# Performance work log

Hardware: AMD Instinct MI355X
Metric: run time of the kernel (lower is better)

Reference implementation:

```python
import jax, jax.numpy as jnp
import numpy as np

B, T, D, H, OUT_STEPS = 4096, 50, 64, 128, 100  # batch, warmup steps, latent dim, hidden units, rollout steps


def setup_inputs() -> dict:
    key = jax.random.key(0)
    ks = jax.random.split(key, 9)
    s = jnp.float32(0.05)  # keep gates out of saturation
    return {
        "x":   jax.random.normal(ks[0], (B, T, D), jnp.float32),
        "Wk0": jax.random.normal(ks[1], (D, 4 * H), jnp.float32) * s,
        "Wr0": jax.random.normal(ks[2], (H, 4 * H), jnp.float32) * s,
        "b0":  jax.random.normal(ks[3], (4 * H,), jnp.float32) * s,
        "Wk1": jax.random.normal(ks[4], (H, 4 * H), jnp.float32) * s,
        "Wr1": jax.random.normal(ks[5], (H, 4 * H), jnp.float32) * s,
        "b1":  jax.random.normal(ks[6], (4 * H,), jnp.float32) * s,
        "Wd":  jax.random.normal(ks[7], (H, D), jnp.float32) * s,
        "bd":  jax.random.normal(ks[8], (D,), jnp.float32) * s,
    }


def _lstm_cell(xt, h, c, Wk, Wr, b):
    # Keras LSTMCell: gates in order i, f, g(cell), o
    z = xt @ Wk + h @ Wr + b  # [B, 4H]
    i, f, g, o = jnp.split(z, 4, axis=-1)
    c_new = jax.nn.sigmoid(f) * c + jax.nn.sigmoid(i) * jnp.tanh(g)
    h_new = jax.nn.sigmoid(o) * jnp.tanh(c_new)
    return h_new, c_new


def reference(x, Wk0, Wr0, b0, Wk1, Wr1, b1, Wd, bd):
    Bn = x.shape[0]
    Hn = Wr0.shape[0]
    z = jnp.zeros((Bn, Hn), x.dtype)

    def warm_step(carry, xt):
        h0, c0, h1, c1 = carry
        h0, c0 = _lstm_cell(xt, h0, c0, Wk0, Wr0, b0)
        h1, c1 = _lstm_cell(h0, h1, c1, Wk1, Wr1, b1)
        return (h0, c0, h1, c1), None

    # warmup over the provided sequence (T >= min_warmup_steps=10)
    carry, _ = jax.lax.scan(warm_step, (z, z, z, z), jnp.swapaxes(x, 0, 1))
    pred0 = carry[2] @ Wd + bd  # Dense on last layer's hidden state

    def ar_step(carry, _):
        pred, h0, c0, h1, c1 = carry
        h0, c0 = _lstm_cell(pred, h0, c0, Wk0, Wr0, b0)
        h1, c1 = _lstm_cell(h0, h1, c1, Wk1, Wr1, b1)
        pred = h1 @ Wd + bd
        return (pred, h0, c0, h1, c1), pred

    _, preds = jax.lax.scan(ar_step, (pred0,) + carry, None, length=OUT_STEPS - 1)
    preds = jnp.concatenate([pred0[None], preds], axis=0)  # [OUT, B, D]
    return jnp.swapaxes(preds, 0, 1)  # [B, OUT, D]
```

## Files before the change

kernel.cpp:

```cpp
#include <hip/hip_runtime.h>
#include <hip/hip_bf16.h>

#define Tt   50
#define Dd   64
#define NOUT 100
#define G4   512
#define K0S  72
#define K1P  264
#define BM   16

typedef __attribute__((ext_vector_type(8))) short  short8;
typedef __attribute__((ext_vector_type(4))) float  floatx4;

#if __has_builtin(__builtin_amdgcn_exp2f)
#define EXP2(v) __builtin_amdgcn_exp2f(v)
#else
#define EXP2(v) exp2f(v)
#endif
__device__ __forceinline__ float rcp_(float v) { return __builtin_amdgcn_rcpf(v); }
#define KN2L2E (-2.8853900817779268f)

#define BARRIER() asm volatile("s_waitcnt lgkmcnt(0)\n\ts_barrier" ::: "memory")

__device__ __forceinline__ short f2bf(float f) {
    __hip_bfloat16 h = __float2bfloat16(f);
    return *reinterpret_cast<const short*>(&h);
}

#define W1F_OFF 196608
#define WDF_OFF 458752
#define B0F_OFF 475136
#define B1F_OFF 477184
#define BDF_OFF 479232

__global__ __launch_bounds__(256) void prep_kernel(
    const float* __restrict__ Wk0, const float* __restrict__ Wr0, const float* __restrict__ b0,
    const float* __restrict__ Wk1, const float* __restrict__ Wr1, const float* __restrict__ b1,
    const float* __restrict__ Wd,  const float* __restrict__ bd,  char* __restrict__ ws)
{
    int idx = blockIdx.x * 256 + threadIdx.x;
    short* w0f = (short*)ws;
    short* w1f = (short*)(ws + W1F_OFF);
    short* wdf = (short*)(ws + WDF_OFF);
    float* b0f = (float*)(ws + B0F_OFF);
    float* b1f = (float*)(ws + B1F_OFF);
    float* bdf = (float*)(ws + BDF_OFF);
    const float NL2E = -1.4426950408889634f;
    const float N2L2E = -2.8853900817779268f;

    if (idx < 98304) {
        int f = idx >> 9, r = idx & 511;
        int lane = r >> 3, j = r & 7;
        int nt = f / 6, kt = f - nt * 6;
        int k = kt * 32 + (lane >> 4) * 8 + j;
        int col = nt * 16 + (lane & 15);
        float sc = ((col >> 7) == 2) ? N2L2E : NL2E;
        w0f[idx] = f2bf(sc * ((k < Dd) ? Wk0[k * G4 + col] : Wr0[(k - Dd) * G4 + col]));
    } else if (idx < 229376) {
        int i2 = idx - 98304;
        int f = i2 >> 9, r = i2 & 511;
        int lane = r >> 3, j = r & 7;
        int nt = f >> 3, kt = f & 7;
        int k = kt * 32 + (lane >> 4) * 8 + j;
        int col = nt * 16 + (lane & 15);
        float sc = ((col >> 7) == 2) ? N2L2E : NL2E;
        w1f[i2] = f2bf(sc * ((k < 128) ? Wk1[k * G4 + col] : Wr1[(k - 128) * G4 + col]));
    } else if (idx < 237568) {
        int i2 = idx - 229376;
        int f = i2 >> 9, r = i2 & 511;
        int lane = r >> 3, j = r & 7;
        int nt = f >> 2, kt = f & 3;
        int k = kt * 32 + (lane >> 4) * 8 + j;
        int col = nt * 16 + (lane & 15);
        wdf[i2] = f2bf(Wd[k * Dd + col]);
    } else if (idx < 237568 + 1088) {
        int i2 = idx - 237568;
        if (i2 < 512) {
            float sc = ((i2 >> 7) == 2) ? N2L2E : NL2E;
            b0f[i2] = sc * b0[i2];
        } else if (i2 < 1024) {
            int c = i2 - 512;
            float sc = ((c >> 7) == 2) ? N2L2E : NL2E;
            b1f[c] = sc * b1[c];
        } else bdf[i2 - 1024] = bd[i2 - 1024];
    }
}

#define SM_A1  4608
#define SM_W0  21504
#define SM_TOT 152576
#define A0SZ   1152
#define A1SZ   4224

#define MFMA_B16(A, B, C) __builtin_amdgcn_mfma_f32_16x16x32_bf16((A), (B), (C), 0, 0, 0)

#define GATES(ACC, CS, BASE, COLOFF)                                                     \
    _Pragma("unroll")                                                                    \
    for (int rr = 0; rr < 4; ++rr) {                                                     \
        float Ei = EXP2(ACC[0][rr]);                                                     \
        float Ef = EXP2(ACC[1][rr]);                                                     \
        float Eg = EXP2(ACC[2][rr]);                                                     \
        float Eo = EXP2(ACC[3][rr]);                                                     \
        float ig = (1.0f - Eg) * rcp_((1.0f + Ei) * (1.0f + Eg));                        \
        float c_ = fmaf(rcp_(1.0f + Ef), CS[rr], ig);                                    \
        CS[rr] = c_;                                                                     \
        float Ec = EXP2(c_ * KN2L2E);                                                    \
        float h_ = (1.0f - Ec) * rcp_((1.0f + Eo) * (1.0f + Ec));                        \
        (BASE)[(quad * 4 + rr) * K1P + (COLOFF) + hu] = f2bf(h_);                        \
    }

__global__ __launch_bounds__(512, 2) void lstm_kernel(
    const float* __restrict__ x, const char* __restrict__ ws, float* __restrict__ out)
{
    extern __shared__ char smem[];
    short* a0b = (short*)smem;
    short* a1b = (short*)(smem + SM_A1);
    short* w0l = (short*)(smem + SM_W0);

    const short* w0f = (const short*)ws;
    const short* w1f = (const short*)(ws + W1F_OFF);
    const short* wdf = (const short*)(ws + WDF_OFF);
    const float* b0f = (const float*)(ws + B0F_OFF);
    const float* b1f = (const float*)(ws + B1F_OFF);
    const float* bdf = (const float*)(ws + BDF_OFF);

    const int tid  = threadIdx.x;
    const int w    = tid >> 6;
    const int lane = tid & 63;
    const int l15  = lane & 15;
    const int quad = lane >> 4;
    const int row0 = blockIdx.x * BM;

    for (int i = tid; i < 2 * A0SZ; i += 512) a0b[i] = 0;
    for (int i = tid; i < 2 * A1SZ; i += 512) a1b[i] = 0;
    for (int c = tid; c < 8192; c += 512) {
        int e8 = c & 63;
        int wv = (c >> 6) & 7;
        int p  = c >> 9;
        int g = p / 6, kt = p - g * 6;
        const short* src = w0f + ((((g * 8 + wv) * 6) + kt) << 9) + e8 * 8;
        *(short8*)&w0l[((p * 8 + wv) << 9) + e8 * 8] = *(const short8*)src;
    }
    {
        int colx = tid & 63, rg = tid >> 6;
        a0b[rg * K0S + colx]       = f2bf(x[(size_t)(row0 + rg) * (Tt * Dd) + colx]);
        a0b[(rg + 8) * K0S + colx] = f2bf(x[(size_t)(row0 + rg + 8) * (Tt * Dd) + colx]);
    }

    const short* w0rb = w0f + w * 3072 + lane * 8;
    const short* w1rb = w1f + w * 4096 + lane * 8;
    short8 W1R[4][8];
    #pragma unroll
    for (int g = 0; g < 4; ++g)
        #pragma unroll
        for (int kt = 0; kt < 8; ++kt)
            W1R[g][kt] = *(const short8*)(w1rb + g * 32768 + kt * 512);
    short8 W0R[8];
    #pragma unroll
    for (int p = 16; p < 24; ++p) {
        int g = p / 6, kt = p - g * 6;
        W0R[p - 16] = *(const short8*)(w0rb + g * 24576 + kt * 512);
    }
    short8 WdR[4];
    if (w < 4) {
        #pragma unroll
        for (int kt = 0; kt < 4; ++kt)
            WdR[kt] = *(const short8*)(wdf + ((w * 4 + kt) << 9) + lane * 8);
    }

    const int hu = w * 16 + l15;
    const float bi0 = b0f[hu], bff0 = b0f[128 + hu], bg0 = b0f[256 + hu], bo0 = b0f[384 + hu];
    const float bi1 = b1f[hu], bff1 = b1f[128 + hu], bg1 = b1f[256 + hu], bo1 = b1f[384 + hu];
    const float bdv = bdf[(w & 3) * 16 + l15];

    float c0s[4] = {0.f, 0.f, 0.f, 0.f};
    float c1s[4] = {0.f, 0.f, 0.f, 0.f};

    const int colx = tid & 63, rg = tid >> 6;

    __syncthreads();

    for (int step = 0; step < 149; ++step) {
        const int p = step & 1, q = p ^ 1;
        short* a0p = a0b + p * A0SZ;  short* a0q = a0b + q * A0SZ;
        short* a1p = a1b + p * A1SZ;  short* a1q = a1b + q * A1SZ;

        float xv0, xv1;
        if (step < Tt - 1) {
            xv0 = x[(size_t)(row0 + rg)     * (Tt * Dd) + (step + 1) * Dd + colx];
            xv1 = x[(size_t)(row0 + rg + 8) * (Tt * Dd) + (step + 1) * Dd + colx];
        }

        floatx4 acc[4];
        acc[0] = (floatx4){bi0,  bi0,  bi0,  bi0};
        acc[1] = (floatx4){bff0, bff0, bff0, bff0};
        acc[2] = (floatx4){bg0,  bg0,  bg0,  bg0};
        acc[3] = (floatx4){bo0,  bo0,  bo0,  bo0};

        #pragma unroll
        for (int kt = 0; kt < 6; ++kt) {
            short8 af = (kt < 2)
                ? *(const short8*)&a0p[l15 * K0S + kt * 32 + quad * 8]
                : *(const short8*)&a1q[l15 * K1P + (kt - 2) * 32 + quad * 8];
            #pragma unroll
            for (int g = 0; g < 4; ++g) {
                const int pp = g * 6 + kt;
                short8 bfr = (pp < 16) ? *(const short8*)&w0l[((pp * 8 + w) << 9) + lane * 8]
                                       : W0R[pp - 16];
                acc[g] = MFMA_B16(af, bfr, acc[g]);
            }
        }

        GATES(acc, c0s, a1p, 0);

        if (step < Tt - 1) {
            a0q[rg * K0S + colx]       = f2bf(xv0);
            a0q[(rg + 8) * K0S + colx] = f2bf(xv1);
        }
        BARRIER();

        acc[0] = (floatx4){bi1,  bi1,  bi1,  bi1};
        acc[1] = (floatx4){bff1, bff1, bff1, bff1};
        acc[2] = (floatx4){bg1,  bg1,  bg1,  bg1};
        acc[3] = (floatx4){bo1,  bo1,  bo1,  bo1};

        #pragma unroll
        for (int kt = 0; kt < 8; ++kt) {
            short8 af = *(const short8*)&a1p[l15 * K1P + kt * 32 + quad * 8];
            #pragma unroll
            for (int g = 0; g < 4; ++g)
                acc[g] = MFMA_B16(af, W1R[g][kt], acc[g]);
        }

        GATES(acc, c1s, a1q, 128);

        if (step >= Tt - 1) {
            BARRIER();
            if (w < 4) {
                floatx4 ad = (floatx4){bdv, bdv, bdv, bdv};
                #pragma unroll
                for (int kt = 0; kt < 4; ++kt) {
                    short8 a_ = *(const short8*)&a1q[l15 * K1P + 128 + kt * 32 + quad * 8];
                    ad = MFMA_B16(a_, WdR[kt], ad);
                }
                int s = step - (Tt - 1);
                #pragma unroll
                for (int r = 0; r < 4; ++r) {
                    float pv = ad[r];
                    int row = quad * 4 + r;
                    int col = w * 16 + l15;
                    out[(size_t)(row0 + row) * (NOUT * Dd) + s * Dd + col] = pv;
                    a0q[row * K0S + col] = f2bf(pv);
                }
            }
            BARRIER();
        }
    }
}

extern "C" void kernel_launch(void* const* d_in, const int* in_sizes, int n_in,
                              void* d_out, int out_size, void* d_ws, size_t ws_size,
                              hipStream_t stream)
{
    (void)in_sizes; (void)n_in; (void)out_size; (void)ws_size;
    static_assert(SM_TOT <= 160 * 1024, "LDS budget");
    hipFuncSetAttribute(reinterpret_cast<const void*>(lstm_kernel),
                        hipFuncAttributeMaxDynamicSharedMemorySize, SM_TOT);
    prep_kernel<<<933, 256, 0, stream>>>(
        (const float*)d_in[1], (const float*)d_in[2], (const float*)d_in[3],
        (const float*)d_in[4], (const float*)d_in[5], (const float*)d_in[6],
        (const float*)d_in[7], (const float*)d_in[8], (char*)d_ws);
    lstm_kernel<<<256, 512, SM_TOT, stream>>>(
        (const float*)d_in[0], (const char*)d_ws, (float*)d_out);
}
```

Before: 479.9 us.

## Precompute layer-0 recurrent term early to overlap with the dense-output barrier

In the autoregressive phase, the h0·Wr0 part of layer-0 gates for the next step is now computed right after layer 1, before the barrier and dense projection. The next step then only needs the two pred·Wk0 k-tiles. This moves recurrent MFMA work off the critical path that waits for the prediction feedback. The accumulator is kept live across the barrier and dense section, which raises register pressure at two blocks per CU.

```diff
diff --git a/kernel.cpp b/kernel.cpp
--- a/kernel.cpp
+++ b/kernel.cpp
@@ -109,6 +109,12 @@
         (BASE)[(quad * 4 + rr) * K1P + (COLOFF) + hu] = f2bf(h_);                        \
     }
 
+#define ACC_INIT(ACC, B0_, B1_, B2_, B3_)            \
+    ACC[0] = (floatx4){B0_, B0_, B0_, B0_};          \
+    ACC[1] = (floatx4){B1_, B1_, B1_, B1_};          \
+    ACC[2] = (floatx4){B2_, B2_, B2_, B2_};          \
+    ACC[3] = (floatx4){B3_, B3_, B3_, B3_};
+
 __global__ __launch_bounds__(512, 2) void lstm_kernel(
     const float* __restrict__ x, const char* __restrict__ ws, float* __restrict__ out)
 {
@@ -142,9 +148,9 @@
         *(short8*)&w0l[((p * 8 + wv) << 9) + e8 * 8] = *(const short8*)src;
     }
     {
-        int colx = tid & 63, rg = tid >> 6;
-        a0b[rg * K0S + colx]       = f2bf(x[(size_t)(row0 + rg) * (Tt * Dd) + colx]);
-        a0b[(rg + 8) * K0S + colx] = f2bf(x[(size_t)(row0 + rg + 8) * (Tt * Dd) + colx]);
+        int cx = tid & 63, rg = tid >> 6;
+        a0b[rg * K0S + cx]       = f2bf(x[(size_t)(row0 + rg) * (Tt * Dd) + cx]);
+        a0b[(rg + 8) * K0S + cx] = f2bf(x[(size_t)(row0 + rg + 8) * (Tt * Dd) + cx]);
     }
 
     const short* w0rb = w0f + w * 3072 + lane * 8;
@@ -180,6 +186,8 @@
 
     __syncthreads();
 
+    floatx4 acc[4];
+
     for (int step = 0; step < 149; ++step) {
         const int p = step & 1, q = p ^ 1;
         short* a0p = a0b + p * A0SZ;  short* a0q = a0b + q * A0SZ;
@@ -191,23 +199,32 @@
             xv1 = x[(size_t)(row0 + rg + 8) * (Tt * Dd) + (step + 1) * Dd + colx];
         }
 
-        floatx4 acc[4];
-        acc[0] = (floatx4){bi0,  bi0,  bi0,  bi0};
-        acc[1] = (floatx4){bff0, bff0, bff0, bff0};
-        acc[2] = (floatx4){bg0,  bg0,  bg0,  bg0};
-        acc[3] = (floatx4){bo0,  bo0,  bo0,  bo0};
-
-        #pragma unroll
-        for (int kt = 0; kt < 6; ++kt) {
-            short8 af = (kt < 2)
-                ? *(const short8*)&a0p[l15 * K0S + kt * 32 + quad * 8]
-                : *(const short8*)&a1q[l15 * K1P + (kt - 2) * 32 + quad * 8];
+        if (step < 50) {
+            ACC_INIT(acc, bi0, bff0, bg0, bo0);
             #pragma unroll
-            for (int g = 0; g < 4; ++g) {
-                const int pp = g * 6 + kt;
-                short8 bfr = (pp < 16) ? *(const short8*)&w0l[((pp * 8 + w) << 9) + lane * 8]
-                                       : W0R[pp - 16];
-                acc[g] = MFMA_B16(af, bfr, acc[g]);
+            for (int kt = 0; kt < 6; ++kt) {
+                short8 af = (kt < 2)
+                    ? *(const short8*)&a0p[l15 * K0S + kt * 32 + quad * 8]
+                    : *(const short8*)&a1q[l15 * K1P + (kt - 2) * 32 + quad * 8];
+                #pragma unroll
+                for (int g = 0; g < 4; ++g) {
+                    const int pp = g * 6 + kt;
+                    short8 bfr = (pp < 16) ? *(const short8*)&w0l[((pp * 8 + w) << 9) + lane * 8]
+                                           : W0R[pp - 16];
+                    acc[g] = MFMA_B16(af, bfr, acc[g]);
+                }
+            }
+        } else {
+            #pragma unroll
+            for (int kt = 0; kt < 2; ++kt) {
+                short8 af = *(const short8*)&a0p[l15 * K0S + kt * 32 + quad * 8];
+                #pragma unroll
+                for (int g = 0; g < 4; ++g) {
+                    const int pp = g * 6 + kt;
+                    short8 bfr = (pp < 16) ? *(const short8*)&w0l[((pp * 8 + w) << 9) + lane * 8]
+                                           : W0R[pp - 16];
+                    acc[g] = MFMA_B16(af, bfr, acc[g]);
+                }
             }
         }
 
@@ -219,11 +236,7 @@
         }
         BARRIER();
 
-        acc[0] = (floatx4){bi1,  bi1,  bi1,  bi1};
-        acc[1] = (floatx4){bff1, bff1, bff1, bff1};
-        acc[2] = (floatx4){bg1,  bg1,  bg1,  bg1};
-        acc[3] = (floatx4){bo1,  bo1,  bo1,  bo1};
-
+        ACC_INIT(acc, bi1, bff1, bg1, bo1);
         #pragma unroll
         for (int kt = 0; kt < 8; ++kt) {
             short8 af = *(const short8*)&a1p[l15 * K1P + kt * 32 + quad * 8];
@@ -235,6 +248,20 @@
         GATES(acc, c1s, a1q, 128);
 
         if (step >= Tt - 1) {
+            if (step < 148) {
+                ACC_INIT(acc, bi0, bff0, bg0, bo0);
+                #pragma unroll
+                for (int kt = 2; kt < 6; ++kt) {
+                    short8 af = *(const short8*)&a1p[l15 * K1P + (kt - 2) * 32 + quad * 8];
+                    #pragma unroll
+                    for (int g = 0; g < 4; ++g) {
+                        const int pp = g * 6 + kt;
+                        short8 bfr = (pp < 16) ? *(const short8*)&w0l[((pp * 8 + w) << 9) + lane * 8]
+                                               : W0R[pp - 16];
+                        acc[g] = MFMA_B16(af, bfr, acc[g]);
+                    }
+                }
+            }
             BARRIER();
             if (w < 4) {
                 floatx4 ad = (floatx4){bdv, bdv, bdv, bdv};
```

Measured after the change: 524.3 us. 9.3% more time.
